# Performance work log

Measured on AMD Instinct MI355X. Metric: run time of the kernel, lower is better.

The kernel has to match this reference:

```python
import jax, jax.numpy as jnp
import numpy as np

K, D_AMB, D_LAT = 16, 512, 10   # k clusters, ambient dim D, latent dim d
B = 16384                       # batch size
LAMB = 0.01                     # objective regularization weight (default)


def setup_inputs() -> dict:
    key = jax.random.key(0)
    k1, k2, k3 = jax.random.split(key, 3)
    std = 0.1 / np.sqrt(D_AMB)  # reset_parameters: normal(0, 0.1/sqrt(D))
    x = jax.random.normal(k1, (B, D_AMB), dtype=jnp.float32)
    Us = (jax.random.normal(k2, (K, D_AMB, D_LAT), dtype=jnp.float32) * std)
    Vs = (jax.random.normal(k3, (K, D_LAT, D_AMB), dtype=jnp.float32) * std)
    return {"x": x, "Us": Us, "Vs": Vs}


def reference(x, Us, Vs):
    # encode: z[k,b,:] = Vs[k] @ x[b]          (k, B, d)
    z = jnp.einsum('kdD,bD->kbd', Vs, x)
    # decode: x_[k,b,:] = Us[k] @ z[k,b]       (k, B, D)
    x_ = jnp.einsum('kDd,kbd->kbD', Us, z)
    # l2_sqr reconstruction loss, reduced over D, transposed to (B, k)
    diff = x[None, :, :] - x_
    loss = jnp.sum(diff * diff, axis=2).T                      # (B, K)
    # subspace regularization per cluster
    reg = 0.5 * (jnp.sum(Us ** 2, axis=(1, 2))
                 + jnp.sum(Vs ** 2, axis=(1, 2)))              # (K,)
    # hard assignment (soft_assign=0): one-hot argmin of detached assign_obj
    assign_obj = jax.lax.stop_gradient(loss + LAMB * reg[None, :])
    c = jax.nn.one_hot(jnp.argmin(assign_obj, axis=1), K, dtype=loss.dtype)
    # objective: mean over batch of c-weighted loss + lamb * c-weighted reg
    loss_term = jnp.mean(jnp.sum(c * loss, axis=1))
    reg_term = LAMB * jnp.mean(jnp.sum(c * reg[None, :], axis=1))
    return loss_term + reg_term
```

## Files before the change

### kernel.cpp

```cpp
#include <hip/hip_runtime.h>


#define KCLUST   16
#define DAMB     512
#define DLAT     10
#define BATCH    16384
#define NC       320
#define LAMBDA   0.01f

#define BM       32
#define NTHREADS 256
#define NKS      16
#define NNT      20
#define YS       325
#define NBLK     (BATCH / BM)
#define PF       4

typedef __attribute__((ext_vector_type(8))) short short8;
typedef __attribute__((ext_vector_type(4))) float f32x4;

__device__ inline short f2bf(float f) {
    unsigned u = __builtin_bit_cast(unsigned, f);
    unsigned r = (u + 0x7FFFu + ((u >> 16) & 1u)) >> 16;
    return (short)r;
}

__global__ __launch_bounds__(256) void setup_k(const float* __restrict__ Us,
                                               const float* __restrict__ Vs,
                                               short* __restrict__ wpack,
                                               float* __restrict__ G,
                                               float* __restrict__ lreg,
                                               unsigned* __restrict__ cnt) {
    int b = blockIdx.x;
    int tid = threadIdx.x;
    if (b == 0 && tid == 0)
        __hip_atomic_store(cnt, 0u, __ATOMIC_RELEASE, __HIP_MEMORY_SCOPE_AGENT);
    if (b < 80) {
        int idx  = b * 256 + tid;
        int ks   = idx / (NNT * 64);
        int rem  = idx % (NNT * 64);
        int nt   = rem / 64;
        int lane = rem % 64;
        int col  = nt * 16 + (lane & 15);
        int cl   = col / 20;
        int c    = col % 20;
        short8 sv;
#pragma unroll
        for (int j = 0; j < 8; ++j) {
            int k = ks * 32 + (lane >> 4) * 8 + j;
            float v;
            if (c < DLAT) v = Vs[(size_t)cl * DLAT * DAMB + c * DAMB + k];
            else          v = Us[(size_t)cl * DAMB * DLAT + k * DLAT + (c - DLAT)];
            sv[j] = f2bf(v);
        }
        *(short8*)&wpack[(size_t)idx * 8] = sv;
    } else {
        __shared__ float red[256];
        int k = b - 80;
        const float* Uk = Us + (size_t)k * DAMB * DLAT;
        const float* Vk = Vs + (size_t)k * DLAT * DAMB;
        float s = 0.f;
        for (int i = tid; i < DAMB * DLAT; i += 256) {
            float a = Uk[i], bb = Vk[i];
            s += a * a + bb * bb;
        }
        red[tid] = s;
        __syncthreads();
        for (int st = 128; st > 0; st >>= 1) {
            if (tid < st) red[tid] += red[tid + st];
            __syncthreads();
        }
        if (tid == 0) lreg[k] = LAMBDA * 0.5f * red[0];
        if (tid < DLAT * DLAT) {
            int i = tid / DLAT, j = tid % DLAT;
            float g = 0.f;
            for (int Dv = 0; Dv < DAMB; ++Dv)
                g += Uk[Dv * DLAT + i] * Uk[Dv * DLAT + j];
            G[k * 100 + tid] = g;
        }
    }
}

__global__ __launch_bounds__(NTHREADS, 2) void main_k(const float* __restrict__ x,
                                                      const short* __restrict__ wpack,
                                                      const float* __restrict__ G,
                                                      const float* __restrict__ lreg,
                                                      float* __restrict__ parts,
                                                      unsigned* __restrict__ cnt,
                                                      float* __restrict__ out) {
    __shared__ __align__(16) char uni[BM * YS * 4];
    __shared__ float Gs[KCLUST * 100];
    __shared__ float lregs[KCLUST];
    __shared__ float rsqp[BM][8];
    __shared__ float rowsq_s[BM];
    __shared__ float objl[BM][17];
    __shared__ float red[NTHREADS];
    __shared__ int   isLast;

    short* a_lds = (short*)uni;
    float* y     = (float*)uni;

    const int tid  = threadIdx.x;
    const int lane = tid & 63;
    const int wv   = tid >> 6;
    const int row0 = blockIdx.x * BM;

    {
        const int srow = tid >> 3;
        const int sc   = tid & 7;
        const int mt   = srow >> 4;
        const int rlo  = srow & 15;
        const float* xr = x + (size_t)(row0 + srow) * DAMB;
        float rs = 0.f;
#pragma unroll
        for (int i = 0; i < 8; ++i) {
            int k8 = sc + 8 * i;
            float4 v0 = *(const float4*)(xr + k8 * 8);
            float4 v1 = *(const float4*)(xr + k8 * 8 + 4);
            rs += v0.x * v0.x + v0.y * v0.y + v0.z * v0.z + v0.w * v0.w
                + v1.x * v1.x + v1.y * v1.y + v1.z * v1.z + v1.w * v1.w;
            short8 sv;
            sv[0] = f2bf(v0.x); sv[1] = f2bf(v0.y); sv[2] = f2bf(v0.z); sv[3] = f2bf(v0.w);
            sv[4] = f2bf(v1.x); sv[5] = f2bf(v1.y); sv[6] = f2bf(v1.z); sv[7] = f2bf(v1.w);
            int ks = k8 >> 2, lh = k8 & 3;
            int ln = (lh << 4) | rlo;
            *(short8*)&a_lds[((mt * NKS + ks) * 64 + ln) * 8] = sv;
        }
        rsqp[srow][sc] = rs;
    }
    for (int i = tid; i < KCLUST * 100; i += NTHREADS) Gs[i] = G[i];
    if (tid < KCLUST) lregs[tid] = lreg[tid];
    __syncthreads();
    if (tid < BM) {
        float s = 0.f;
#pragma unroll
        for (int j = 0; j < 8; ++j) s += rsqp[tid][j];
        rowsq_s[tid] = s;
    }

    f32x4 acc[2][5];
#pragma unroll
    for (int m = 0; m < 2; ++m)
#pragma unroll
        for (int j = 0; j < 5; ++j) acc[m][j] = (f32x4)0.f;

    const short8* wp8 = (const short8*)wpack;
    short8 bbuf[PF][5];
#pragma unroll
    for (int p = 0; p < PF; ++p)
#pragma unroll
        for (int j = 0; j < 5; ++j)
            bbuf[p][j] = wp8[(p * NNT + wv * 5 + j) * 64 + lane];

    short8 a0 = *(short8*)&a_lds[((0 * NKS + 0) * 64 + lane) * 8];
    short8 a1 = *(short8*)&a_lds[((1 * NKS + 0) * 64 + lane) * 8];

#pragma unroll
    for (int ks = 0; ks < NKS; ++ks) {
        short8 b0 = bbuf[ks & (PF - 1)][0], b1 = bbuf[ks & (PF - 1)][1],
               b2 = bbuf[ks & (PF - 1)][2], b3 = bbuf[ks & (PF - 1)][3],
               b4 = bbuf[ks & (PF - 1)][4];
        if (ks + PF < NKS) {
#pragma unroll
            for (int j = 0; j < 5; ++j)
                bbuf[ks & (PF - 1)][j] = wp8[((ks + PF) * NNT + wv * 5 + j) * 64 + lane];
        }
        short8 na0 = a0, na1 = a1;
        if (ks + 1 < NKS) {
            na0 = *(short8*)&a_lds[((0 * NKS + ks + 1) * 64 + lane) * 8];
            na1 = *(short8*)&a_lds[((1 * NKS + ks + 1) * 64 + lane) * 8];
        }
        acc[0][0] = __builtin_amdgcn_mfma_f32_16x16x32_bf16(a0, b0, acc[0][0], 0, 0, 0);
        acc[1][0] = __builtin_amdgcn_mfma_f32_16x16x32_bf16(a1, b0, acc[1][0], 0, 0, 0);
        acc[0][1] = __builtin_amdgcn_mfma_f32_16x16x32_bf16(a0, b1, acc[0][1], 0, 0, 0);
        acc[1][1] = __builtin_amdgcn_mfma_f32_16x16x32_bf16(a1, b1, acc[1][1], 0, 0, 0);
        acc[0][2] = __builtin_amdgcn_mfma_f32_16x16x32_bf16(a0, b2, acc[0][2], 0, 0, 0);
        acc[1][2] = __builtin_amdgcn_mfma_f32_16x16x32_bf16(a1, b2, acc[1][2], 0, 0, 0);
        acc[0][3] = __builtin_amdgcn_mfma_f32_16x16x32_bf16(a0, b3, acc[0][3], 0, 0, 0);
        acc[1][3] = __builtin_amdgcn_mfma_f32_16x16x32_bf16(a1, b3, acc[1][3], 0, 0, 0);
        acc[0][4] = __builtin_amdgcn_mfma_f32_16x16x32_bf16(a0, b4, acc[0][4], 0, 0, 0);
        acc[1][4] = __builtin_amdgcn_mfma_f32_16x16x32_bf16(a1, b4, acc[1][4], 0, 0, 0);
        a0 = na0; a1 = na1;
    }
    __syncthreads();

#pragma unroll
    for (int m = 0; m < 2; ++m) {
        int rowb = m * 16 + (lane >> 4) * 4;
#pragma unroll
        for (int j = 0; j < 5; ++j) {
            int colb = (wv * 5 + j) * 16 + (lane & 15);
#pragma unroll
            for (int r = 0; r < 4; ++r)
                y[(rowb + r) * YS + colb] = acc[m][j][r];
        }
    }
    __syncthreads();

#pragma unroll
    for (int it = 0; it < 2; ++it) {
        int row = tid & 31;
        int kk  = (tid >> 5) + 8 * it;
        const float* yy = y + row * YS + kk * 20;
        float z[DLAT], w[DLAT];
#pragma unroll
        for (int i = 0; i < DLAT; ++i) { z[i] = yy[i]; w[i] = yy[DLAT + i]; }
        const float* Gk = Gs + kk * 100;
        float s = 0.f, wz = 0.f;
#pragma unroll
        for (int i = 0; i < DLAT; ++i) {
            float gz = 0.f;
#pragma unroll
            for (int j = 0; j < DLAT; ++j) gz = fmaf(Gk[i * DLAT + j], z[j], gz);
            s  = fmaf(z[i], gz, s);
            wz = fmaf(w[i], z[i], wz);
        }
        objl[row][kk] = s - 2.f * wz + lregs[kk];
    }
    __syncthreads();

    if (wv == 0) {
        float v = 0.f;
        if (lane < BM) {
            float m = objl[lane][0];
#pragma unroll
            for (int k = 1; k < KCLUST; ++k) m = fminf(m, objl[lane][k]);
            v = m + rowsq_s[lane];
        }
#pragma unroll
        for (int off = 32; off > 0; off >>= 1) v += __shfl_down(v, off);
        if (lane == 0) {
            __hip_atomic_store(&parts[blockIdx.x], v, __ATOMIC_RELEASE,
                               __HIP_MEMORY_SCOPE_AGENT);
            unsigned prev = __hip_atomic_fetch_add(cnt, 1u, __ATOMIC_ACQ_REL,
                                                   __HIP_MEMORY_SCOPE_AGENT);
            isLast = (prev == NBLK - 1);
        }
    }
    __syncthreads();

    if (isLast) {
        float s = __hip_atomic_load(&parts[tid], __ATOMIC_RELAXED, __HIP_MEMORY_SCOPE_AGENT)
                + __hip_atomic_load(&parts[tid + NTHREADS], __ATOMIC_RELAXED, __HIP_MEMORY_SCOPE_AGENT);
        red[tid] = s;
        __syncthreads();
        for (int st = NTHREADS / 2; st > 0; st >>= 1) {
            if (tid < st) red[tid] += red[tid + st];
            __syncthreads();
        }
        if (tid == 0) out[0] = red[0] * (1.0f / BATCH);
    }
}

extern "C" void kernel_launch(void* const* d_in, const int* in_sizes, int n_in,
                              void* d_out, int out_size, void* d_ws, size_t ws_size,
                              hipStream_t stream) {
    const float* x  = (const float*)d_in[0];
    const float* Us = (const float*)d_in[1];
    const float* Vs = (const float*)d_in[2];
    float* out = (float*)d_out;

    short* wpack   = (short*)d_ws;
    float* G       = (float*)(wpack + NKS * NNT * 64 * 8);
    float* lreg    = G + KCLUST * 100;
    float* parts   = lreg + KCLUST;
    unsigned* cnt  = (unsigned*)(parts + NBLK);

    setup_k<<<96, 256, 0, stream>>>(Us, Vs, wpack, G, lreg, cnt);
    main_k<<<NBLK, NTHREADS, 0, stream>>>(x, wpack, G, lreg, parts, cnt, out);
}
```

Baseline: 54.57 us.

## Halve rows per block to 16 and double occupancy target

Each block now handles 16 rows instead of 32, which doubles the grid to 1024 blocks and raises the launch bounds to 4 blocks per SM. Each wave issues 5 MFMAs per k-step instead of 10, with a single A operand loaded directly from LDS, and the weight prefetch depth drops from 4 to 2. The aim is more parallelism and latency hiding across a larger grid with less shared memory per block. The cost is that every block reloads the full packed weight matrix, so global weight traffic doubles and B-operand reuse per block halves.

```diff
diff --git a/kernel.cpp b/kernel.cpp
--- a/kernel.cpp
+++ b/kernel.cpp
@@ -8,13 +8,13 @@
 #define NC       320
 #define LAMBDA   0.01f
 
-#define BM       32
+#define BM       16
 #define NTHREADS 256
 #define NKS      16
 #define NNT      20
 #define YS       325
 #define NBLK     (BATCH / BM)
-#define PF       4
+#define PF       2
 
 typedef __attribute__((ext_vector_type(8))) short short8;
 typedef __attribute__((ext_vector_type(4))) float f32x4;
@@ -81,7 +81,7 @@
     }
 }
 
-__global__ __launch_bounds__(NTHREADS, 2) void main_k(const float* __restrict__ x,
+__global__ __launch_bounds__(NTHREADS, 4) void main_k(const float* __restrict__ x,
                                                       const short* __restrict__ wpack,
                                                       const float* __restrict__ G,
                                                       const float* __restrict__ lreg,
@@ -91,7 +91,7 @@
     __shared__ __align__(16) char uni[BM * YS * 4];
     __shared__ float Gs[KCLUST * 100];
     __shared__ float lregs[KCLUST];
-    __shared__ float rsqp[BM][8];
+    __shared__ float rsqp[BM][16];
     __shared__ float rowsq_s[BM];
     __shared__ float objl[BM][17];
     __shared__ float red[NTHREADS];
@@ -106,25 +106,23 @@
     const int row0 = blockIdx.x * BM;
 
     {
-        const int srow = tid >> 3;
-        const int sc   = tid & 7;
-        const int mt   = srow >> 4;
-        const int rlo  = srow & 15;
+        const int srow = tid >> 4;
+        const int sc   = tid & 15;
         const float* xr = x + (size_t)(row0 + srow) * DAMB;
         float rs = 0.f;
 #pragma unroll
-        for (int i = 0; i < 8; ++i) {
-            int k8 = sc + 8 * i;
-            float4 v0 = *(const float4*)(xr + k8 * 8);
-            float4 v1 = *(const float4*)(xr + k8 * 8 + 4);
+        for (int i = 0; i < 4; ++i) {
+            int g = sc + 16 * i;
+            float4 v0 = *(const float4*)(xr + g * 8);
+            float4 v1 = *(const float4*)(xr + g * 8 + 4);
             rs += v0.x * v0.x + v0.y * v0.y + v0.z * v0.z + v0.w * v0.w
                 + v1.x * v1.x + v1.y * v1.y + v1.z * v1.z + v1.w * v1.w;
             short8 sv;
             sv[0] = f2bf(v0.x); sv[1] = f2bf(v0.y); sv[2] = f2bf(v0.z); sv[3] = f2bf(v0.w);
             sv[4] = f2bf(v1.x); sv[5] = f2bf(v1.y); sv[6] = f2bf(v1.z); sv[7] = f2bf(v1.w);
-            int ks = k8 >> 2, lh = k8 & 3;
-            int ln = (lh << 4) | rlo;
-            *(short8*)&a_lds[((mt * NKS + ks) * 64 + ln) * 8] = sv;
+            int ks = g >> 2, lh = g & 3;
+            int ln = (lh << 4) | srow;
+            *(short8*)&a_lds[(ks * 64 + ln) * 8] = sv;
         }
         rsqp[srow][sc] = rs;
     }
@@ -134,15 +132,13 @@
     if (tid < BM) {
         float s = 0.f;
 #pragma unroll
-        for (int j = 0; j < 8; ++j) s += rsqp[tid][j];
+        for (int j = 0; j < 16; ++j) s += rsqp[tid][j];
         rowsq_s[tid] = s;
     }
 
-    f32x4 acc[2][5];
-#pragma unroll
-    for (int m = 0; m < 2; ++m)
-#pragma unroll
-        for (int j = 0; j < 5; ++j) acc[m][j] = (f32x4)0.f;
+    f32x4 acc[5];
+#pragma unroll
+    for (int j = 0; j < 5; ++j) acc[j] = (f32x4)0.f;
 
     const short8* wp8 = (const short8*)wpack;
     short8 bbuf[PF][5];
@@ -151,9 +147,6 @@
 #pragma unroll
         for (int j = 0; j < 5; ++j)
             bbuf[p][j] = wp8[(p * NNT + wv * 5 + j) * 64 + lane];
-
-    short8 a0 = *(short8*)&a_lds[((0 * NKS + 0) * 64 + lane) * 8];
-    short8 a1 = *(short8*)&a_lds[((1 * NKS + 0) * 64 + lane) * 8];
 
 #pragma unroll
     for (int ks = 0; ks < NKS; ++ks) {
@@ -165,42 +158,30 @@
             for (int j = 0; j < 5; ++j)
                 bbuf[ks & (PF - 1)][j] = wp8[((ks + PF) * NNT + wv * 5 + j) * 64 + lane];
         }
-        short8 na0 = a0, na1 = a1;
-        if (ks + 1 < NKS) {
-            na0 = *(short8*)&a_lds[((0 * NKS + ks + 1) * 64 + lane) * 8];
-            na1 = *(short8*)&a_lds[((1 * NKS + ks + 1) * 64 + lane) * 8];
-        }
-        acc[0][0] = __builtin_amdgcn_mfma_f32_16x16x32_bf16(a0, b0, acc[0][0], 0, 0, 0);
-        acc[1][0] = __builtin_amdgcn_mfma_f32_16x16x32_bf16(a1, b0, acc[1][0], 0, 0, 0);
-        acc[0][1] = __builtin_amdgcn_mfma_f32_16x16x32_bf16(a0, b1, acc[0][1], 0, 0, 0);
-        acc[1][1] = __builtin_amdgcn_mfma_f32_16x16x32_bf16(a1, b1, acc[1][1], 0, 0, 0);
-        acc[0][2] = __builtin_amdgcn_mfma_f32_16x16x32_bf16(a0, b2, acc[0][2], 0, 0, 0);
-        acc[1][2] = __builtin_amdgcn_mfma_f32_16x16x32_bf16(a1, b2, acc[1][2], 0, 0, 0);
-        acc[0][3] = __builtin_amdgcn_mfma_f32_16x16x32_bf16(a0, b3, acc[0][3], 0, 0, 0);
-        acc[1][3] = __builtin_amdgcn_mfma_f32_16x16x32_bf16(a1, b3, acc[1][3], 0, 0, 0);
-        acc[0][4] = __builtin_amdgcn_mfma_f32_16x16x32_bf16(a0, b4, acc[0][4], 0, 0, 0);
-        acc[1][4] = __builtin_amdgcn_mfma_f32_16x16x32_bf16(a1, b4, acc[1][4], 0, 0, 0);
-        a0 = na0; a1 = na1;
-    }
-    __syncthreads();
-
-#pragma unroll
-    for (int m = 0; m < 2; ++m) {
-        int rowb = m * 16 + (lane >> 4) * 4;
+        short8 a0 = *(short8*)&a_lds[(ks * 64 + lane) * 8];
+        acc[0] = __builtin_amdgcn_mfma_f32_16x16x32_bf16(a0, b0, acc[0], 0, 0, 0);
+        acc[1] = __builtin_amdgcn_mfma_f32_16x16x32_bf16(a0, b1, acc[1], 0, 0, 0);
+        acc[2] = __builtin_amdgcn_mfma_f32_16x16x32_bf16(a0, b2, acc[2], 0, 0, 0);
+        acc[3] = __builtin_amdgcn_mfma_f32_16x16x32_bf16(a0, b3, acc[3], 0, 0, 0);
+        acc[4] = __builtin_amdgcn_mfma_f32_16x16x32_bf16(a0, b4, acc[4], 0, 0, 0);
+    }
+    __syncthreads();
+
+    {
+        int rowb = (lane >> 4) * 4;
 #pragma unroll
         for (int j = 0; j < 5; ++j) {
             int colb = (wv * 5 + j) * 16 + (lane & 15);
 #pragma unroll
             for (int r = 0; r < 4; ++r)
-                y[(rowb + r) * YS + colb] = acc[m][j][r];
-        }
-    }
-    __syncthreads();
-
-#pragma unroll
-    for (int it = 0; it < 2; ++it) {
-        int row = tid & 31;
-        int kk  = (tid >> 5) + 8 * it;
+                y[(rowb + r) * YS + colb] = acc[j][r];
+        }
+    }
+    __syncthreads();
+
+    {
+        int kk  = tid >> 4;
+        int row = tid & 15;
         const float* yy = y + row * YS + kk * 20;
         float z[DLAT], w[DLAT];
 #pragma unroll
@@ -228,7 +209,7 @@
             v = m + rowsq_s[lane];
         }
 #pragma unroll
-        for (int off = 32; off > 0; off >>= 1) v += __shfl_down(v, off);
+        for (int off = 8; off > 0; off >>= 1) v += __shfl_down(v, off);
         if (lane == 0) {
             __hip_atomic_store(&parts[blockIdx.x], v, __ATOMIC_RELEASE,
                                __HIP_MEMORY_SCOPE_AGENT);
@@ -240,8 +221,11 @@
     __syncthreads();
 
     if (isLast) {
-        float s = __hip_atomic_load(&parts[tid], __ATOMIC_RELAXED, __HIP_MEMORY_SCOPE_AGENT)
-                + __hip_atomic_load(&parts[tid + NTHREADS], __ATOMIC_RELAXED, __HIP_MEMORY_SCOPE_AGENT);
+        float s = 0.f;
+#pragma unroll
+        for (int q = 0; q < NBLK / NTHREADS; ++q)
+            s += __hip_atomic_load(&parts[tid + q * NTHREADS], __ATOMIC_RELAXED,
+                                   __HIP_MEMORY_SCOPE_AGENT);
         red[tid] = s;
         __syncthreads();
         for (int st = NTHREADS / 2; st > 0; st >>= 1) {
```

After: 65.37 us. 19.8% more time.
